# Kernel tuning notes

Measured on AMD Instinct MI355X. Metric: run time of the kernel, lower is better.

The kernel has to match this reference:

```python
import jax, jax.numpy as jnp
import numpy as np

D_IN = 1024
D_OUT = 1024
NUM_HEADS = 16
HEAD_DIM = D_OUT // NUM_HEADS


def setup_inputs() -> dict:
    key = jax.random.key(0)
    k1, k2, k3, k4 = jax.random.split(key, 4)
    x = jax.random.normal(k1, (2, 2048, D_IN), dtype=jnp.float32)
    # qkv Linear (bias=False): weight [3*d_out, d_in]
    w_qkv = jax.random.normal(k2, (3 * D_OUT, D_IN), dtype=jnp.float32) * (1.0 / np.sqrt(D_IN))
    # proj Linear (default bias=True): weight [d_out, d_out], bias [d_out]
    w_proj = jax.random.normal(k3, (D_OUT, D_OUT), dtype=jnp.float32) * (1.0 / np.sqrt(D_OUT))
    b_proj = jax.random.normal(k4, (D_OUT,), dtype=jnp.float32) * 0.01
    return {"x": x, "w_qkv": w_qkv, "w_proj": w_proj, "b_proj": b_proj}


def reference(x, w_qkv, w_proj, b_proj):
    B, S, E = x.shape
    qkv = jnp.einsum("bse,fe->bsf", x, w_qkv)                 # [B,S,3*d_out]
    qkv = qkv.reshape(B, S, 3, NUM_HEADS, HEAD_DIM)
    qkv = jnp.transpose(qkv, (2, 0, 3, 1, 4))                  # [3,B,H,S,D]
    q, k, v = qkv[0], qkv[1], qkv[2]
    scores = jnp.einsum("bhqd,bhkd->bhqk", q, k)               # [B,H,S,S]
    causal = jnp.triu(jnp.ones((S, S), dtype=bool), k=1)
    scores = jnp.where(causal, -jnp.inf, scores)
    # NOTE: source divides by head_dim**(-0.5), i.e. multiplies by sqrt(head_dim)
    scores = scores / (HEAD_DIM ** -0.5)
    attn = jax.nn.softmax(scores, axis=-1)
    ctx = jnp.einsum("bhqk,bhkd->bhqd", attn, v)               # [B,H,S,D]
    ctx = jnp.transpose(ctx, (0, 2, 1, 3)).reshape(B, S, E)
    return jnp.einsum("bse,fe->bsf", ctx, w_proj) + b_proj
```

## Files before the change

### kernel.cpp

```cpp
#include <hip/hip_runtime.h>

typedef _Float16 f16;
typedef _Float16 f16x4 __attribute__((ext_vector_type(4)));
typedef _Float16 f16x8 __attribute__((ext_vector_type(8)));
typedef float f32x4 __attribute__((ext_vector_type(4)));

#define MFMA16(a, b, c) __builtin_amdgcn_mfma_f32_16x16x32_f16(a, b, c, 0, 0, 0)
#define QSCALE 11.5415603f

typedef const __attribute__((address_space(1))) void* gp1_t;
typedef __attribute__((address_space(3))) void* lp3_t;
__device__ __forceinline__ void gld16(const void* g, void* l) {
    __builtin_amdgcn_global_load_lds((gp1_t)g, (lp3_t)l, 16, 0, 0);
}

__device__ __forceinline__ int unit_nc(int j)     { return j < 22 ? 1 : (j < 44 ? 2 : 3); }
__device__ __forceinline__ int unit_prefix(int j) { return j < 22 ? j : (j < 44 ? 22 + 2 * (j - 22) : 66 + 3 * (j - 44)); }

__global__ __launch_bounds__(256) void cvt_all(
    const float* __restrict__ x, const float* __restrict__ wq, const float* __restrict__ wp,
    f16* __restrict__ xh, f16* __restrict__ wqh, f16* __restrict__ wph)
{
    int i = blockIdx.x * 256 + threadIdx.x;
    const float4* src; f16x4* dst; int off;
    if (i < 1048576)      { src = (const float4*)x;  dst = (f16x4*)xh;  off = i; }
    else if (i < 1835008) { src = (const float4*)wq; dst = (f16x4*)wqh; off = i - 1048576; }
    else                  { src = (const float4*)wp; dst = (f16x4*)wph; off = i - 1835008; }
    float4 v = src[off];
    f16x4 o = { (f16)v.x, (f16)v.y, (f16)v.z, (f16)v.w };
    dst[off] = o;
}

template<int EPI>
__global__ __launch_bounds__(256) void gemm_k(
    const f16* __restrict__ A, const f16* __restrict__ B, int K,
    f16* __restrict__ qb, f16* __restrict__ kb, f16* __restrict__ vt,
    float* __restrict__ outF, const float* __restrict__ bias)
{
    __shared__ f16 as[128 * 32];
    __shared__ f16 bs[128 * 32];
    const int t = threadIdx.x;
    const int m0 = blockIdx.y * 128, n0 = blockIdx.x * 128;
    const int lane = t & 63, wv = t >> 6;
    const int wm = wv >> 1, wn = wv & 1;
    const int lr = lane & 15, g = lane >> 4;
    const int srow = lane >> 2, schk = (lane & 3) * 8;
    const f16* Ab = A + (size_t)m0 * K;
    const f16* Bb = B + (size_t)n0 * K;
    f32x4 acc[4][4] = {};

    for (int k0 = 0; k0 < K; k0 += 32) {
        __syncthreads();
        #pragma unroll
        for (int i2 = 0; i2 < 2; ++i2) {
            const int r0 = wv * 32 + i2 * 16;
            gld16(&Ab[(size_t)(r0 + srow) * K + k0 + schk], &as[r0 * 32]);
            gld16(&Bb[(size_t)(r0 + srow) * K + k0 + schk], &bs[r0 * 32]);
        }
        __syncthreads();
        f16x8 af[4], bf[4];
        #pragma unroll
        for (int mt = 0; mt < 4; ++mt)
            af[mt] = *reinterpret_cast<const f16x8*>(&as[(wm * 64 + mt * 16 + lr) * 32 + g * 8]);
        #pragma unroll
        for (int nt = 0; nt < 4; ++nt)
            bf[nt] = *reinterpret_cast<const f16x8*>(&bs[(wn * 64 + nt * 16 + lr) * 32 + g * 8]);
        #pragma unroll
        for (int mt = 0; mt < 4; ++mt)
            #pragma unroll
            for (int nt = 0; nt < 4; ++nt)
                acc[mt][nt] = MFMA16(af[mt], bf[nt], acc[mt][nt]);
    }

    #pragma unroll
    for (int mt = 0; mt < 4; ++mt) {
        #pragma unroll
        for (int nt = 0; nt < 4; ++nt) {
            const int n = n0 + wn * 64 + nt * 16 + lr;
            const int s0 = m0 + wm * 64 + mt * 16 + 4 * g;
            if (EPI == 0) {
                const int which = n >> 10, h = (n >> 6) & 15, d = n & 63;
                const int b = s0 >> 11, s = s0 & 2047;
                if (which == 2) {
                    f16x4 vv;
                    #pragma unroll
                    for (int i = 0; i < 4; ++i) vv[i] = (f16)acc[mt][nt][i];
                    *reinterpret_cast<f16x4*>(&vt[((size_t)((b << 4) + h) * 64 + d) * 2048 + s]) = vv;
                } else {
                    f16* dst = which ? kb : qb;
                    const float sc = which ? 1.0f : QSCALE;
                    #pragma unroll
                    for (int i = 0; i < 4; ++i)
                        dst[((size_t)((b << 4) + h) * 2048 + (s + i)) * 64 + d] = (f16)(acc[mt][nt][i] * sc);
                }
            } else {
                #pragma unroll
                for (int i = 0; i < 4; ++i)
                    outF[(size_t)(s0 + i) * 1024 + n] = acc[mt][nt][i] + bias[n];
            }
        }
    }
}

__global__ __launch_bounds__(64) void attn_k(
    const f16* __restrict__ Q, const f16* __restrict__ K, const f16* __restrict__ VT,
    f16* __restrict__ opart, float* __restrict__ mpart, float* __restrict__ lpart)
{
    __shared__ f16 lp[32][72];
    const int lane = threadIdx.x;
    const int lr = lane & 15, g = lane >> 4;
    const int bid = blockIdx.x;
    const int bh = bid & 31;
    const int rest = bid >> 5;
    const int j = 63 - rest / 3;
    const int c = rest % 3;
    const int ntt = (j >> 1) + 1;
    const int nc = unit_nc(j);
    if (c >= nc) return;
    const int cbase = ntt / nc, crem = ntt - cbase * nc;
    const int start = c * cbase + (c < crem ? c : crem);
    const int len = cbase + (c < crem ? 1 : 0);
    const bool diag = (start + len == ntt);

    const size_t base = (size_t)bh * (2048 * 64);
    const f16* Qb = Q + base;
    const f16* Kb = K + base;
    const f16* Vb = VT + base;
    const int q0 = j << 5;

    f16x8 qf[2][2];
    #pragma unroll
    for (int nt = 0; nt < 2; ++nt)
        #pragma unroll
        for (int ks = 0; ks < 2; ++ks)
            qf[nt][ks] = *reinterpret_cast<const f16x8*>(&Qb[(size_t)(q0 + nt * 16 + lr) * 64 + ks * 32 + g * 8]);

    f32x4 o[4][2] = {};
    float mrun[2] = { -1e30f, -1e30f };
    float lsum[2] = { 0.f, 0.f };

#define ATTN_TILE(KV0, MTMAX, MASKED) do {                                              \
    const int kv0_ = (KV0);                                                             \
    f32x4 st[MTMAX][2] = {};                                                            \
    _Pragma("unroll")                                                                   \
    for (int mt = 0; mt < MTMAX; ++mt) {                                                \
        f16x8 ak[2];                                                                    \
        _Pragma("unroll")                                                               \
        for (int ks = 0; ks < 2; ++ks)                                                  \
            ak[ks] = *reinterpret_cast<const f16x8*>(                                   \
                &Kb[(size_t)(kv0_ + mt * 16 + lr) * 64 + ks * 32 + g * 8]);             \
        _Pragma("unroll")                                                               \
        for (int nt = 0; nt < 2; ++nt)                                                  \
            _Pragma("unroll")                                                           \
            for (int ks = 0; ks < 2; ++ks)                                              \
                st[mt][nt] = MFMA16(ak[ks], qf[nt][ks], st[mt][nt]);                    \
    }                                                                                   \
    _Pragma("unroll")                                                                   \
    for (int nt = 0; nt < 2; ++nt) {                                                    \
        const int qrow_ = q0 + nt * 16 + lr;                                            \
        float mloc = -1e30f;                                                            \
        _Pragma("unroll")                                                               \
        for (int mt = 0; mt < MTMAX; ++mt)                                              \
            _Pragma("unroll")                                                           \
            for (int i = 0; i < 4; ++i) {                                               \
                float sv = st[mt][nt][i];                                               \
                if (MASKED) {                                                           \
                    int kkk = kv0_ + mt * 16 + 4 * g + i;                               \
                    sv = (kkk <= qrow_) ? sv : -1e30f;                                  \
                    st[mt][nt][i] = sv;                                                 \
                }                                                                       \
                mloc = fmaxf(mloc, sv);                                                 \
            }                                                                           \
        mloc = fmaxf(mloc, __shfl_xor(mloc, 16));                                       \
        mloc = fmaxf(mloc, __shfl_xor(mloc, 32));                                       \
        if (__any(mloc > mrun[nt] + 8.0f)) {                             \
            float mnew = fmaxf(mrun[nt], mloc);                                         \
            float sc = exp2f(mrun[nt] - mnew);                                          \
            lsum[nt] *= sc;                                                             \
            _Pragma("unroll")                                                           \
            for (int mo = 0; mo < 4; ++mo)                                              \
                _Pragma("unroll")                                                       \
                for (int i = 0; i < 4; ++i) o[mo][nt][i] *= sc;                         \
            mrun[nt] = mnew;                                                            \
        }                                                                               \
        float ls = 0.f;                                                                 \
        _Pragma("unroll")                                                               \
        for (int mt = 0; mt < MTMAX; ++mt) {                                            \
            f16x4 pk;                                                                   \
            _Pragma("unroll")                                                           \
            for (int i = 0; i < 4; ++i) {                                               \
                float p = exp2f(st[mt][nt][i] - mrun[nt]);                              \
                ls += p; pk[i] = (f16)p;                                                \
            }                                                                           \
            *reinterpret_cast<f16x4*>(&lp[nt * 16 + lr][mt * 16 + 4 * g]) = pk;         \
        }                                                                               \
        lsum[nt] += ls;                                                                 \
    }                                                                                   \
    {                                                                                   \
        constexpr int PVKS = (MTMAX) / 2;                                               \
        f16x8 pf[2][PVKS];                                                              \
        _Pragma("unroll")                                                               \
        for (int nt = 0; nt < 2; ++nt)                                                  \
            _Pragma("unroll")                                                           \
            for (int ks = 0; ks < PVKS; ++ks)                                           \
                pf[nt][ks] = *reinterpret_cast<const f16x8*>(                           \
                    &lp[nt * 16 + lr][ks * 32 + g * 8]);                                \
        _Pragma("unroll")                                                               \
        for (int mo = 0; mo < 4; ++mo) {                                                \
            f16x8 av[PVKS];                                                             \
            _Pragma("unroll")                                                           \
            for (int ks = 0; ks < PVKS; ++ks)                                           \
                av[ks] = *reinterpret_cast<const f16x8*>(                               \
                    &Vb[(size_t)(mo * 16 + lr) * 2048 + kv0_ + ks * 32 + g * 8]);       \
            _Pragma("unroll")                                                           \
            for (int nt = 0; nt < 2; ++nt)                                              \
                _Pragma("unroll")                                                       \
                for (int ks = 0; ks < PVKS; ++ks)                                       \
                    o[mo][nt] = MFMA16(av[ks], pf[nt][ks], o[mo][nt]);                  \
        }                                                                               \
    }                                                                                   \
} while (0)

    const int tEnd = start + len - (diag ? 1 : 0);
    for (int tt = start; tt < tEnd; ++tt)
        ATTN_TILE(tt << 6, 4, false);
    if (diag) {
        const int kvl = (ntt - 1) << 6;
        if (j & 1) ATTN_TILE(kvl, 4, true);
        else       ATTN_TILE(kvl, 2, true);
    }
#undef ATTN_TILE

    const int slot = bh * 126 + unit_prefix(j) + c;
    #pragma unroll
    for (int nt = 0; nt < 2; ++nt) {
        float l = lsum[nt];
        l += __shfl_xor(l, 16);
        l += __shfl_xor(l, 32);
        const float inv = 1.0f / l;
        const int ql = nt * 16 + lr;
        const int mi = slot * 32 + ql;
        #pragma unroll
        for (int mo = 0; mo < 4; ++mo) {
            f16x4 ov;
            #pragma unroll
            for (int i = 0; i < 4; ++i) ov[i] = (f16)(o[mo][nt][i] * inv);
            *reinterpret_cast<f16x4*>(&opart[(size_t)mi * 64 + mo * 16 + 4 * g]) = ov;
        }
        if (g == 0) { mpart[mi] = mrun[nt]; lpart[mi] = l; }
    }
}

__global__ __launch_bounds__(256) void combine_k(
    const f16* __restrict__ opart, const float* __restrict__ mpart,
    const float* __restrict__ lpart, f16* __restrict__ ctx)
{
    const int blk = blockIdx.x;
    const int bh = blk & 31, j = blk >> 5;
    const int b = bh >> 4, h = bh & 15;
    const int nc = unit_nc(j);
    const int slot0 = bh * 126 + unit_prefix(j);
    const int t = threadIdx.x;
    const int q = t >> 3, dc = (t & 7) * 8;

    float m[3], l[3];
    float M = -1e30f;
    for (int cc = 0; cc < nc; ++cc) {
        m[cc] = mpart[(slot0 + cc) * 32 + q];
        l[cc] = lpart[(slot0 + cc) * 32 + q];
        M = fmaxf(M, m[cc]);
    }
    float wsum = 0.f, w[3];
    for (int cc = 0; cc < nc; ++cc) { w[cc] = l[cc] * exp2f(m[cc] - M); wsum += w[cc]; }
    const float r = 1.0f / wsum;

    float acc[8] = {};
    for (int cc = 0; cc < nc; ++cc) {
        const float coef = w[cc] * r;
        f16x8 v = *reinterpret_cast<const f16x8*>(&opart[(size_t)((slot0 + cc) * 32 + q) * 64 + dc]);
        #pragma unroll
        for (int i = 0; i < 8; ++i) acc[i] += coef * (float)v[i];
    }
    f16x8 outv;
    #pragma unroll
    for (int i = 0; i < 8; ++i) outv[i] = (f16)acc[i];
    const int qg = j * 32 + q;
    *reinterpret_cast<f16x8*>(&ctx[((size_t)(b * 2048 + qg)) * 1024 + h * 64 + dc]) = outv;
}

extern "C" void kernel_launch(void* const* d_in, const int* in_sizes, int n_in,
                              void* d_out, int out_size, void* d_ws, size_t ws_size,
                              hipStream_t stream) {
    const float* x      = (const float*)d_in[0];
    const float* w_qkv  = (const float*)d_in[1];
    const float* w_proj = (const float*)d_in[2];
    const float* b_proj = (const float*)d_in[3];
    float* out = (float*)d_out;

    char* p = (char*)d_ws;
    f16* xh     = (f16*)p; p += (size_t)4096 * 1024 * 2;
    f16* wqkvh  = (f16*)p; p += (size_t)3072 * 1024 * 2;
    f16* wprojh = (f16*)p; p += (size_t)1024 * 1024 * 2;
    f16* qbuf   = (f16*)p; p += (size_t)2 * 16 * 2048 * 64 * 2;
    f16* kbuf   = (f16*)p; p += (size_t)2 * 16 * 2048 * 64 * 2;
    f16* vtbuf  = (f16*)p; p += (size_t)2 * 16 * 64 * 2048 * 2;
    f16* ctx    = (f16*)p; p += (size_t)4096 * 1024 * 2;

    f16*   opart = (f16*)d_out;
    float* mpart = (float*)xh;
    float* lpart = mpart + 129024;

    cvt_all<<<8192, 256, 0, stream>>>(x, w_qkv, w_proj, xh, wqkvh, wprojh);

    gemm_k<0><<<dim3(24, 32), 256, 0, stream>>>(xh, wqkvh, 1024, qbuf, kbuf, vtbuf, nullptr, nullptr);

    attn_k<<<6144, 64, 0, stream>>>(qbuf, kbuf, vtbuf, opart, mpart, lpart);

    combine_k<<<2048, 256, 0, stream>>>(opart, mpart, lpart, ctx);

    gemm_k<1><<<dim3(8, 32), 256, 0, stream>>>(ctx, wprojh, 1024, nullptr, nullptr, nullptr, out, b_proj);
}
```

Before: 222.2 us.

## Enlarge attention query tile to 64 rows and write unsplit units directly to ctx

The attention kernel now processes 64 query rows per wave instead of 32, so each K/V tile loaded is reused across twice as many queries. The KV split schedule is rebuilt around 32 units with up to 4 splits. Units that are not split write normalized output straight into ctx, and the combine kernel runs only for split units. The diagonal tile skips MFMAs above the causal diagonal. In exchange the kernel uses more registers per wave and launches fewer, larger blocks.

Measured after the change: 199.5 us. -10.2%, faster.

```diff
diff --git a/kernel.cpp b/kernel.cpp
--- a/kernel.cpp
+++ b/kernel.cpp
@@ -13,9 +13,6 @@
 __device__ __forceinline__ void gld16(const void* g, void* l) {
     __builtin_amdgcn_global_load_lds((gp1_t)g, (lp3_t)l, 16, 0, 0);
 }
-
-__device__ __forceinline__ int unit_nc(int j)     { return j < 22 ? 1 : (j < 44 ? 2 : 3); }
-__device__ __forceinline__ int unit_prefix(int j) { return j < 22 ? j : (j < 44 ? 22 + 2 * (j - 22) : 66 + 3 * (j - 44)); }
 
 __global__ __launch_bounds__(256) void cvt_all(
     const float* __restrict__ x, const float* __restrict__ wq, const float* __restrict__ wp,
@@ -102,75 +99,81 @@
     }
 }
 
-__global__ __launch_bounds__(64) void attn_k(
+__global__ __launch_bounds__(64, 2) void attn_k(
     const f16* __restrict__ Q, const f16* __restrict__ K, const f16* __restrict__ VT,
-    f16* __restrict__ opart, float* __restrict__ mpart, float* __restrict__ lpart)
+    f16* __restrict__ ctx, f16* __restrict__ opart,
+    float* __restrict__ mpart, float* __restrict__ lpart)
 {
-    __shared__ f16 lp[32][72];
+    __shared__ f16 lp[64][72];
     const int lane = threadIdx.x;
     const int lr = lane & 15, g = lane >> 4;
     const int bid = blockIdx.x;
     const int bh = bid & 31;
-    const int rest = bid >> 5;
-    const int j = 63 - rest / 3;
-    const int c = rest % 3;
-    const int ntt = (j >> 1) + 1;
-    const int nc = unit_nc(j);
-    if (c >= nc) return;
-    const int cbase = ntt / nc, crem = ntt - cbase * nc;
+    const int rr = 67 - (bid >> 5);
+    int u, c;
+    if (rr < 10)      { u = rr;                 c = 0; }
+    else if (rr < 30) { u = 10 + (rr - 10) / 2; c = (rr - 10) % 2; }
+    else if (rr < 60) { u = 20 + (rr - 30) / 3; c = (rr - 30) % 3; }
+    else              { u = 30 + (rr - 60) / 4; c = (rr - 60) % 4; }
+    const int ntt = u + 1;
+    const int nc  = 1 + u / 10;
+    const int cbase = ntt / nc, crem = ntt % nc;
     const int start = c * cbase + (c < crem ? c : crem);
-    const int len = cbase + (c < crem ? 1 : 0);
+    const int len   = cbase + (c < crem ? 1 : 0);
     const bool diag = (start + len == ntt);
 
+    const int b = bh >> 4, h = bh & 15;
     const size_t base = (size_t)bh * (2048 * 64);
     const f16* Qb = Q + base;
     const f16* Kb = K + base;
     const f16* Vb = VT + base;
-    const int q0 = j << 5;
-
-    f16x8 qf[2][2];
+    const int q0 = u << 6;
+
+    f16x8 qf[4][2];
     #pragma unroll
-    for (int nt = 0; nt < 2; ++nt)
+    for (int nt = 0; nt < 4; ++nt)
         #pragma unroll
         for (int ks = 0; ks < 2; ++ks)
             qf[nt][ks] = *reinterpret_cast<const f16x8*>(&Qb[(size_t)(q0 + nt * 16 + lr) * 64 + ks * 32 + g * 8]);
 
-    f32x4 o[4][2] = {};
-    float mrun[2] = { -1e30f, -1e30f };
-    float lsum[2] = { 0.f, 0.f };
-
-#define ATTN_TILE(KV0, MTMAX, MASKED) do {                                              \
+    f32x4 o[4][4] = {};
+    float mrun[4] = { -1e30f, -1e30f, -1e30f, -1e30f };
+    float lsum[4] = { 0.f, 0.f, 0.f, 0.f };
+
+#define ATTN_TILE(KV0, DIAGM) do {                                                      \
     const int kv0_ = (KV0);                                                             \
-    f32x4 st[MTMAX][2] = {};                                                            \
+    f32x4 st[4][4] = {};                                                                \
     _Pragma("unroll")                                                                   \
-    for (int mt = 0; mt < MTMAX; ++mt) {                                                \
+    for (int mt = 0; mt < 4; ++mt) {                                                    \
         f16x8 ak[2];                                                                    \
         _Pragma("unroll")                                                               \
         for (int ks = 0; ks < 2; ++ks)                                                  \
             ak[ks] = *reinterpret_cast<const f16x8*>(                                   \
                 &Kb[(size_t)(kv0_ + mt * 16 + lr) * 64 + ks * 32 + g * 8]);             \
         _Pragma("unroll")                                                               \
-        for (int nt = 0; nt < 2; ++nt)                                                  \
-            _Pragma("unroll")                                                           \
-            for (int ks = 0; ks < 2; ++ks)                                              \
-                st[mt][nt] = MFMA16(ak[ks], qf[nt][ks], st[mt][nt]);                    \
+        for (int nt = 0; nt < 4; ++nt)                                                  \
+            if (!(DIAGM) || mt <= nt) {                                                 \
+                _Pragma("unroll")                                                       \
+                for (int ks = 0; ks < 2; ++ks)                                          \
+                    st[mt][nt] = MFMA16(ak[ks], qf[nt][ks], st[mt][nt]);                \
+            }                                                                           \
     }                                                                                   \
     _Pragma("unroll")                                                                   \
-    for (int nt = 0; nt < 2; ++nt) {                                                    \
-        const int qrow_ = q0 + nt * 16 + lr;                                            \
+    for (int nt = 0; nt < 4; ++nt) {                                                    \
         float mloc = -1e30f;                                                            \
         _Pragma("unroll")                                                               \
-        for (int mt = 0; mt < MTMAX; ++mt)                                              \
+        for (int mt = 0; mt < 4; ++mt) {                                                \
+            if ((DIAGM) && mt > nt) continue;                                           \
             _Pragma("unroll")                                                           \
             for (int i = 0; i < 4; ++i) {                                               \
                 float sv = st[mt][nt][i];                                               \
-                if (MASKED) {                                                           \
-                    int kkk = kv0_ + mt * 16 + 4 * g + i;                               \
-                    sv = (kkk <= qrow_) ? sv : -1e30f;                                  \
+                if ((DIAGM) && mt == nt) {             \
+                    sv = (4 * g + i <= lr) ? sv : -1e30f;                               \
                     st[mt][nt][i] = sv;                                                 \
                 }                                                                       \
                 mloc = fmaxf(mloc, sv);                                                 \
             }                                                                           \
+        }                                                                               \
         mloc = fmaxf(mloc, __shfl_xor(mloc, 16));                                       \
         mloc = fmaxf(mloc, __shfl_xor(mloc, 32));                                       \
         if (__any(mloc > mrun[nt] + 8.0f)) {                             \
@@ -185,37 +188,40 @@
         }                                                                               \
         float ls = 0.f;                                                                 \
         _Pragma("unroll")                                                               \
-        for (int mt = 0; mt < MTMAX; ++mt) {                                            \
+        for (int mt = 0; mt < 4; ++mt) {                                                \
             f16x4 pk;                                                                   \
-            _Pragma("unroll")                                                           \
-            for (int i = 0; i < 4; ++i) {                                               \
-                float p = exp2f(st[mt][nt][i] - mrun[nt]);                              \
-                ls += p; pk[i] = (f16)p;                                                \
+            if ((DIAGM) && mt > nt) {                                                   \
+                pk[0] = pk[1] = pk[2] = pk[3] = (f16)0.f;                               \
+            } else {                                                                    \
+                _Pragma("unroll")                                                       \
+                for (int i = 0; i < 4; ++i) {                                           \
+                    float p = exp2f(st[mt][nt][i] - mrun[nt]);                          \
+                    ls += p; pk[i] = (f16)p;                                            \
+                }                                                                       \
             }                                                                           \
             *reinterpret_cast<f16x4*>(&lp[nt * 16 + lr][mt * 16 + 4 * g]) = pk;         \
         }                                                                               \
         lsum[nt] += ls;                                                                 \
     }                                                                                   \
     {                                                                                   \
-        constexpr int PVKS = (MTMAX) / 2;                                               \
-        f16x8 pf[2][PVKS];                                                              \
-        _Pragma("unroll")                                                               \
-        for (int nt = 0; nt < 2; ++nt)                                                  \
-            _Pragma("unroll")                                                           \
-            for (int ks = 0; ks < PVKS; ++ks)                                           \
+        f16x8 pf[4][2];                                                                 \
+        _Pragma("unroll")                                                               \
+        for (int nt = 0; nt < 4; ++nt)                                                  \
+            _Pragma("unroll")                                                           \
+            for (int ks = 0; ks < 2; ++ks)                                              \
                 pf[nt][ks] = *reinterpret_cast<const f16x8*>(                           \
                     &lp[nt * 16 + lr][ks * 32 + g * 8]);                                \
         _Pragma("unroll")                                                               \
         for (int mo = 0; mo < 4; ++mo) {                                                \
-            f16x8 av[PVKS];                                                             \
-            _Pragma("unroll")                                                           \
-            for (int ks = 0; ks < PVKS; ++ks)                                           \
+            f16x8 av[2];                                                                \
+            _Pragma("unroll")                                                           \
+            for (int ks = 0; ks < 2; ++ks)                                              \
                 av[ks] = *reinterpret_cast<const f16x8*>(                               \
                     &Vb[(size_t)(mo * 16 + lr) * 2048 + kv0_ + ks * 32 + g * 8]);       \
             _Pragma("unroll")                                                           \
-            for (int nt = 0; nt < 2; ++nt)                                              \
+            for (int nt = 0; nt < 4; ++nt)                                              \
                 _Pragma("unroll")                                                       \
-                for (int ks = 0; ks < PVKS; ++ks)                                       \
+                for (int ks = 0; ks < 2; ++ks)                                          \
                     o[mo][nt] = MFMA16(av[ks], pf[nt][ks], o[mo][nt]);                  \
         }                                                                               \
     }                                                                                   \
@@ -223,31 +229,44 @@
 
     const int tEnd = start + len - (diag ? 1 : 0);
     for (int tt = start; tt < tEnd; ++tt)
-        ATTN_TILE(tt << 6, 4, false);
-    if (diag) {
-        const int kvl = (ntt - 1) << 6;
-        if (j & 1) ATTN_TILE(kvl, 4, true);
-        else       ATTN_TILE(kvl, 2, true);
-    }
+        ATTN_TILE(tt << 6, 0);
+    if (diag)
+        ATTN_TILE((ntt - 1) << 6, 1);
 #undef ATTN_TILE
 
-    const int slot = bh * 126 + unit_prefix(j) + c;
+    const bool split = (nc > 1);
+    int slot = 0;
+    if (split) {
+        const int psl = (u < 20) ? 2 * (u - 10) : (u < 30 ? 20 + 3 * (u - 20) : 50 + 4 * (u - 30));
+        slot = bh * 58 + psl + c;
+    }
     #pragma unroll
-    for (int nt = 0; nt < 2; ++nt) {
+    for (int nt = 0; nt < 4; ++nt) {
         float l = lsum[nt];
         l += __shfl_xor(l, 16);
         l += __shfl_xor(l, 32);
         const float inv = 1.0f / l;
-        const int ql = nt * 16 + lr;
-        const int mi = slot * 32 + ql;
-        #pragma unroll
-        for (int mo = 0; mo < 4; ++mo) {
-            f16x4 ov;
+        const int lrow = nt * 16 + lr;
+        if (!split) {
+            const size_t rowoff = ((size_t)(b * 2048 + q0 + lrow)) * 1024 + h * 64;
             #pragma unroll
-            for (int i = 0; i < 4; ++i) ov[i] = (f16)(o[mo][nt][i] * inv);
-            *reinterpret_cast<f16x4*>(&opart[(size_t)mi * 64 + mo * 16 + 4 * g]) = ov;
+            for (int mo = 0; mo < 4; ++mo) {
+                f16x4 ov;
+                #pragma unroll
+                for (int i = 0; i < 4; ++i) ov[i] = (f16)(o[mo][nt][i] * inv);
+                *reinterpret_cast<f16x4*>(&ctx[rowoff + mo * 16 + 4 * g]) = ov;
+            }
+        } else {
+            const int mi = slot * 64 + lrow;
+            #pragma unroll
+            for (int mo = 0; mo < 4; ++mo) {
+                f16x4 ov;
+                #pragma unroll
+                for (int i = 0; i < 4; ++i) ov[i] = (f16)(o[mo][nt][i] * inv);
+                *reinterpret_cast<f16x4*>(&opart[(size_t)mi * 64 + mo * 16 + 4 * g]) = ov;
+            }
+            if (g == 0) { mpart[mi] = mrun[nt]; lpart[mi] = l; }
         }
-        if (g == 0) { mpart[mi] = mrun[nt]; lpart[mi] = l; }
     }
 }
 
@@ -256,36 +275,43 @@
     const float* __restrict__ lpart, f16* __restrict__ ctx)
 {
     const int blk = blockIdx.x;
-    const int bh = blk & 31, j = blk >> 5;
+    const int bh = blk & 31, u = 10 + (blk >> 5);
     const int b = bh >> 4, h = bh & 15;
-    const int nc = unit_nc(j);
-    const int slot0 = bh * 126 + unit_prefix(j);
+    const int nc = 1 + u / 10;
+    const int psl = (u < 20) ? 2 * (u - 10) : (u < 30 ? 20 + 3 * (u - 20) : 50 + 4 * (u - 30));
+    const int slot0 = bh * 58 + psl;
     const int t = threadIdx.x;
-    const int q = t >> 3, dc = (t & 7) * 8;
-
-    float m[3], l[3];
+    const int lrow = t >> 2, seg = t & 3;
+
+    float m[4], l[4], w[4];
     float M = -1e30f;
-    for (int cc = 0; cc < nc; ++cc) {
-        m[cc] = mpart[(slot0 + cc) * 32 + q];
-        l[cc] = lpart[(slot0 + cc) * 32 + q];
+    #pragma unroll 4
+    for (int cc = 0; cc < 4; ++cc) if (cc < nc) {
+        m[cc] = mpart[(slot0 + cc) * 64 + lrow];
+        l[cc] = lpart[(slot0 + cc) * 64 + lrow];
         M = fmaxf(M, m[cc]);
     }
-    float wsum = 0.f, w[3];
-    for (int cc = 0; cc < nc; ++cc) { w[cc] = l[cc] * exp2f(m[cc] - M); wsum += w[cc]; }
+    float wsum = 0.f;
+    #pragma unroll 4
+    for (int cc = 0; cc < 4; ++cc) if (cc < nc) { w[cc] = l[cc] * exp2f(m[cc] - M); wsum += w[cc]; }
     const float r = 1.0f / wsum;
 
-    float acc[8] = {};
-    for (int cc = 0; cc < nc; ++cc) {
+    float acc[16] = {};
+    #pragma unroll 4
+    for (int cc = 0; cc < 4; ++cc) if (cc < nc) {
         const float coef = w[cc] * r;
-        f16x8 v = *reinterpret_cast<const f16x8*>(&opart[(size_t)((slot0 + cc) * 32 + q) * 64 + dc]);
-        #pragma unroll
-        for (int i = 0; i < 8; ++i) acc[i] += coef * (float)v[i];
-    }
-    f16x8 outv;
+        const size_t rb = (size_t)((slot0 + cc) * 64 + lrow) * 64 + seg * 16;
+        f16x8 v0 = *reinterpret_cast<const f16x8*>(&opart[rb]);
+        f16x8 v1 = *reinterpret_cast<const f16x8*>(&opart[rb + 8]);
+        #pragma unroll
+        for (int i = 0; i < 8; ++i) { acc[i] += coef * (float)v0[i]; acc[i + 8] += coef * (float)v1[i]; }
+    }
+    f16x8 o0, o1;
     #pragma unroll
-    for (int i = 0; i < 8; ++i) outv[i] = (f16)acc[i];
-    const int qg = j * 32 + q;
-    *reinterpret_cast<f16x8*>(&ctx[((size_t)(b * 2048 + qg)) * 1024 + h * 64 + dc]) = outv;
+    for (int i = 0; i < 8; ++i) { o0[i] = (f16)acc[i]; o1[i] = (f16)acc[i + 8]; }
+    const size_t wb = ((size_t)(b * 2048 + u * 64 + lrow)) * 1024 + h * 64 + seg * 16;
+    *reinterpret_cast<f16x8*>(&ctx[wb]) = o0;
+    *reinterpret_cast<f16x8*>(&ctx[wb + 8]) = o1;
 }
 
 extern "C" void kernel_launch(void* const* d_in, const int* in_sizes, int n_in,
@@ -308,15 +334,15 @@
 
     f16*   opart = (f16*)d_out;
     float* mpart = (float*)xh;
-    float* lpart = mpart + 129024;
+    float* lpart = mpart + 118784;
 
     cvt_all<<<8192, 256, 0, stream>>>(x, w_qkv, w_proj, xh, wqkvh, wprojh);
 
     gemm_k<0><<<dim3(24, 32), 256, 0, stream>>>(xh, wqkvh, 1024, qbuf, kbuf, vtbuf, nullptr, nullptr);
 
-    attn_k<<<6144, 64, 0, stream>>>(qbuf, kbuf, vtbuf, opart, mpart, lpart);
-
-    combine_k<<<2048, 256, 0, stream>>>(opart, mpart, lpart, ctx);
+    attn_k<<<2176, 64, 0, stream>>>(qbuf, kbuf, vtbuf, ctx, opart, mpart, lpart);
+
+    combine_k<<<704, 256, 0, stream>>>(opart, mpart, lpart, ctx);
 
     gemm_k<1><<<dim3(8, 32), 256, 0, stream>>>(ctx, wprojh, 1024, nullptr, nullptr, nullptr, out, b_proj);
 }
```
